# Kernel optimization log

Measured on AMD Instinct MI355X. Metric: run time of the kernel, lower is better.

The kernel has to match this reference:

```python
import jax, jax.numpy as jnp
import numpy as np

B, C, V = 65536, 2, 3          # batch of coords, coord_dim, value_dim
D, K, S = 64, 1024, 4          # latent_dim, num_codes, num_latent_vectors (VQ stages)
H, L, F = 1024, 5, 25          # hidden_size, num_layers, num_freqs
IN = C * (2 * F + 1)           # 102: positional-encoded decoder input
COMMIT = 0.25


def setup_inputs() -> dict:
    key = jax.random.key(0)
    ks = jax.random.split(key, 12)
    coords = jax.random.uniform(ks[0], (B, C), jnp.float32, -1.0, 1.0)
    latents = jax.random.normal(ks[1], (1, S, D), jnp.float32)
    cb = jax.random.normal(ks[2], (S, K, D), jnp.float32)
    codebooks = cb / jnp.linalg.norm(cb, axis=-1, keepdims=True)  # unit-norm init as in module
    mod_W = jax.random.normal(ks[3], (L, D, H), jnp.float32) / np.sqrt(D)
    mod_b = jax.random.normal(ks[4], (L, H), jnp.float32) * 0.01
    dec_W0 = jax.random.normal(ks[5], (IN, H), jnp.float32) / np.sqrt(IN)
    dec_b0 = jax.random.normal(ks[6], (H,), jnp.float32) * 0.01
    dec_Wh = jax.random.normal(ks[7], (L - 1, H, H), jnp.float32) / np.sqrt(H)
    dec_bh = jax.random.normal(ks[8], (L - 1, H), jnp.float32) * 0.01
    dec_Wout = jax.random.normal(ks[9], (H, V), jnp.float32) / np.sqrt(H)
    dec_bout = jax.random.normal(ks[10], (V,), jnp.float32) * 0.01
    return dict(coords=coords, latent_idx=0, latents=latents, codebooks=codebooks,
                mod_W=mod_W, mod_b=mod_b, dec_W0=dec_W0, dec_b0=dec_b0,
                dec_Wh=dec_Wh, dec_bh=dec_bh, dec_Wout=dec_Wout, dec_bout=dec_bout)


def _vq(z, emb):
    # z: (1, D), emb: (K, D) -> squared-distance argmin + straight-through
    d = jnp.sum(z * z, axis=1, keepdims=True) - 2.0 * (z @ emb.T) + jnp.sum(emb * emb, axis=1)
    idx = jnp.argmin(d, axis=1)               # (1,)
    z_q = emb[idx]                            # (1, D)
    z_q_st = z_q + jax.lax.stop_gradient(z - z_q)   # fwd value == z, grad flows to embedding
    loss = COMMIT * jnp.mean((jax.lax.stop_gradient(z_q) - z) ** 2)
    return z_q_st, idx, loss


def reference(coords, latent_idx, latents, codebooks, mod_W, mod_b,
              dec_W0, dec_b0, dec_Wh, dec_bh, dec_Wout, dec_bout):
    img = latents[latent_idx]                 # (S, D)
    z_q_sum = jnp.zeros((1, D), coords.dtype)
    residual_target = jnp.zeros((1, D), coords.dtype)
    total_vq_loss = 0.0
    idxs = []
    for s in range(S):                        # residual VQ over fixed small #stages
        z_stage = img[s:s + 1]
        if s == 0:
            residual_target = z_stage
            z_cur = z_stage
        else:
            residual_target = residual_target + z_stage
            z_cur = residual_target - jax.lax.stop_gradient(z_q_sum)
        z_q_st, idx, l = _vq(z_cur, codebooks[s])
        z_q_sum = z_q_sum + z_q_st
        total_vq_loss = total_vq_loss + l
        idxs.append(idx)
    # modulation betas from the (same-for-all-rows) quantized latent; broadcast over B
    betas = jnp.einsum('od,ldh->loh', z_q_sum, mod_W) + mod_b[:, None, :]   # (L, 1, H)
    # positional encoding: [x, sin(pi*f0*x), cos(pi*f0*x), sin(pi*f1*x), ...]
    freqs = 2.0 ** jnp.arange(F, dtype=coords.dtype)
    ang = coords[:, None, :] * (freqs[None, :, None] * jnp.pi)              # (B, F, C)
    pe = jnp.concatenate(
        [coords, jnp.stack([jnp.sin(ang), jnp.cos(ang)], axis=2).reshape(coords.shape[0], -1)],
        axis=-1)                                                            # (B, IN)
    h = jax.nn.relu(pe @ dec_W0 + dec_b0 + betas[0])
    for i in range(L - 1):
        h = jax.nn.relu(h @ dec_Wh[i] + dec_bh[i] + betas[i + 1])
    values = h @ dec_Wout + dec_bout                                        # (B, V)
    return values, jnp.stack(idxs), total_vq_loss
```

## Files before the change

kernel.cpp:

```cpp
#include <hip/hip_runtime.h>
#include <hip/hip_bf16.h>
#include <stdint.h>

#define NB   65536
#define NC   2
#define NV   3
#define ND   64
#define NK   1024
#define NS   4
#define NH   1024
#define NL   5
#define NF   25
#define NIN  102
#define K0P  128

typedef float f32x4 __attribute__((ext_vector_type(4)));
typedef int   i32x4 __attribute__((ext_vector_type(4)));
typedef int   i32x8 __attribute__((ext_vector_type(8)));
typedef unsigned char u8;

__device__ __forceinline__ void load_lds16(const void* g, void* l) {
    __builtin_amdgcn_global_load_lds(
        (const __attribute__((address_space(1))) void*)g,
        (__attribute__((address_space(3))) void*)l,
        16, 0, 0);
}

__device__ __forceinline__ u8 to_fp8(float x) {
    return (u8)(__builtin_amdgcn_cvt_pk_fp8_f32(x, 0.0f, 0, false) & 0xff);
}


__global__ __launch_bounds__(1024) void vq_kernel(
    const float* __restrict__ latents, const int* __restrict__ latent_idx,
    const float* __restrict__ codebooks, float* __restrict__ zq_out,
    float* __restrict__ out) {
    __shared__ float zcur[ND], resid[ND], zqsum[ND], ssq[ND];
    __shared__ float sDw[16];
    __shared__ int   sKw[16];
    __shared__ int   sBest;
    int t = threadIdx.x, lane = t & 63, wv = t >> 6;
    const float* img = latents + (size_t)latent_idx[0] * (NS * ND);
    if (t < ND) { resid[t] = 0.f; zqsum[t] = 0.f; }
    __syncthreads();
    float lossAcc = 0.f;
    for (int s = 0; s < NS; s++) {
        if (t < ND) {
            float iv = img[s * ND + t];
            float r  = resid[t] + iv;
            resid[t] = r;
            zcur[t]  = (s == 0) ? iv : (r - zqsum[t]);
        }
        __syncthreads();
        float zz = 0.f;
#pragma unroll
        for (int d = 0; d < ND; d++) { float z = zcur[d]; zz += z * z; }
        const float4* e4 = (const float4*)(codebooks + ((size_t)s * NK + t) * ND);
        float dot = 0.f, ee = 0.f;
#pragma unroll
        for (int i = 0; i < 16; i++) {
            float4 v = e4[i];
            dot += zcur[4 * i + 0] * v.x; dot += zcur[4 * i + 1] * v.y;
            dot += zcur[4 * i + 2] * v.z; dot += zcur[4 * i + 3] * v.w;
            ee  += v.x * v.x; ee += v.y * v.y; ee += v.z * v.z; ee += v.w * v.w;
        }
        float dmin = zz - 2.0f * dot + ee;
        int   kmin = t;
#pragma unroll
        for (int m = 1; m < 64; m <<= 1) {
            float d2 = __shfl_xor(dmin, m);
            int   k2 = __shfl_xor(kmin, m);
            if (d2 < dmin || (d2 == dmin && k2 < kmin)) { dmin = d2; kmin = k2; }
        }
        if (lane == 0) { sDw[wv] = dmin; sKw[wv] = kmin; }
        __syncthreads();
        if (t == 0) {
            float bd = sDw[0]; int bk = sKw[0];
            for (int w = 1; w < 16; w++) {
                float d2 = sDw[w]; int k2 = sKw[w];
                if (d2 < bd || (d2 == bd && k2 < bk)) { bd = d2; bk = k2; }
            }
            sBest = bk;
            out[NB * NV + s] = (float)bk;
        }
        __syncthreads();
        int best = sBest;
        const float* eb = codebooks + ((size_t)s * NK + best) * ND;
        if (t < ND) {
            float zq = eb[t];
            float d  = zq - zcur[t];
            ssq[t]   = d * d;
            zqsum[t] = zqsum[t] + (zq + (zcur[t] - zq));
        }
        __syncthreads();
        if (t == 0) {
            float sum = 0.f;
            for (int d = 0; d < ND; d++) sum += ssq[d];
            lossAcc += 0.25f * (sum / (float)ND);
        }
    }
    if (t < ND) zq_out[t] = zqsum[t];
    if (t == 0) out[NB * NV + NS] = lossAcc;
}

__global__ __launch_bounds__(256) void betas_kernel(
    const float* __restrict__ zq, const float* __restrict__ mod_W,
    const float* __restrict__ mod_b, const float* __restrict__ b0,
    const float* __restrict__ bh, float* __restrict__ bb) {
    int g = blockIdx.x * 256 + threadIdx.x;
    int l = g >> 10, n = g & 1023;
    float acc = mod_b[g];
    for (int d = 0; d < ND; d++) acc += zq[d] * mod_W[(size_t)(l * ND + d) * NH + n];
    acc += (l == 0) ? b0[n] : bh[(size_t)(l - 1) * NH + n];
    bb[g] = acc;
}

__global__ __launch_bounds__(256) void init_out_kernel(
    const float* __restrict__ bout, float* __restrict__ out) {
    int g = blockIdx.x * 256 + threadIdx.x;
    out[g] = bout[g % NV];
}

__global__ __launch_bounds__(256) void prep_kernel(
    const float* __restrict__ src, u8* __restrict__ dst, int Ks, int Kp) {
    __shared__ float tile[32][33];
    int nIt = Kp >> 7;
    src += (size_t)blockIdx.z * Ks * NH;
    dst += (size_t)blockIdx.z * NH * Kp;
    int k0 = blockIdx.x * 32, n0 = blockIdx.y * 32;
    int tx = threadIdx.x, ty = threadIdx.y;
    for (int i = 0; i < 4; i++) {
        int k = k0 + ty + i * 8;
        int n = n0 + tx;
        tile[ty + i * 8][tx] = (k < Ks) ? src[(size_t)k * NH + n] : 0.0f;
    }
    __syncthreads();
    for (int i = 0; i < 4; i++) {
        int n = n0 + ty + i * 8;
        int k = k0 + tx;
        int bn = n >> 7, j = (n >> 4) & 7, r16 = n & 15;
        int it = k >> 7, q = (k >> 5) & 3, half = (k >> 4) & 1, b16 = k & 15;
        size_t flat = ((size_t)(((bn * nIt + it) * 8 + j) * 2 + half)) * 1024
                    + (q * 16 + r16) * 16 + b16;
        dst[flat] = to_fp8(tile[tx][ty + i * 8] * 64.0f);
    }
}

__device__ __forceinline__ float pe_val(const float* coords, int m, int k) {
    if (k < 2) return coords[m * 2 + k];
    if (k >= NIN) return 0.0f;
    int u = k - 2;
    int f = u >> 2, r = u & 3;
    float c = coords[m * 2 + (r & 1)];
    float a = c * __builtin_ldexpf(3.14159274101257324f, f);
    return (r < 2) ? sinf(a) : cosf(a);
}

__global__ __launch_bounds__(256) void pe_kernel(
    const float* __restrict__ coords, u8* __restrict__ pe) {
    int g = blockIdx.x * 256 + threadIdx.x;
    int m = g >> 5, k4 = (g & 31) * 4;
    float v0 = pe_val(coords, m, k4 + 0);
    float v1 = pe_val(coords, m, k4 + 1);
    float v2 = pe_val(coords, m, k4 + 2);
    float v3 = pe_val(coords, m, k4 + 3);
    int p = __builtin_amdgcn_cvt_pk_fp8_f32(v0, v1, 0, false);
    p     = __builtin_amdgcn_cvt_pk_fp8_f32(v2, v3, p, true);
    int m16 = m >> 4, r = m & 15, c32 = k4 >> 5, b = k4 & 31;
    *(int*)(pe + ((size_t)(m16 * 4 + c32) * 16 + r) * 32 + b) = p;
}

template <int MODE, int KT>
__global__ __launch_bounds__(256, 2) void gemm_kernel(
    const u8* __restrict__ A, const u8* __restrict__ W,
    const float* __restrict__ bb, u8* __restrict__ O,
    const float* __restrict__ Wout, float* __restrict__ out, int Mb) {
    __shared__ __align__(16) u8 smem[32768];
    u8* sW0 = smem;
    u8* sW1 = smem + 16384;
    int t   = threadIdx.x;
    int fid = blockIdx.x;
    int xcd = fid & 7;
    int j8  = fid >> 3;
    int bn  = j8 & 7;
    int bm  = xcd * (Mb >> 3) + (j8 >> 3);
    int lane = t & 63, wm = t >> 6;
    int q    = lane >> 4, r16 = lane & 15;
    const int nIt = KT >> 7;

    const u8* wslab = W + (size_t)(bn * nIt) * 16384;
    const u8* abase = A + ((size_t)(bm * 16 + wm * 4) * (KT >> 5)) * 512 + lane * 32;

    f32x4 acc[4][8];
    f32x4 zero = {0.f, 0.f, 0.f, 0.f};
    for (int i = 0; i < 4; i++)
        for (int j = 0; j < 8; j++) acc[i][j] = zero;

#pragma unroll
    for (int p = 0; p < 4; p++) {
        int g = p * 256 + t;
        load_lds16((const void*)(wslab + g * 16), (void*)(sW0 + g * 16));
    }
    i32x8 afc[4], afn[4];
#pragma unroll
    for (int i = 0; i < 4; i++) {
        const u8* p = abase + ((size_t)i * (KT >> 5)) * 512;
        i32x4 lo = *(const i32x4*)(p);
        i32x4 hi = *(const i32x4*)(p + 16);
        afc[i] = __builtin_shufflevector(lo, hi, 0, 1, 2, 3, 4, 5, 6, 7);
    }
    __syncthreads();

#pragma unroll 1
    for (int it = 0; it < nIt; it++) {
        u8* bufc = (it & 1) ? sW1 : sW0;
        u8* bufn = (it & 1) ? sW0 : sW1;
        if (it + 1 < nIt) {
            const u8* ws = wslab + (size_t)(it + 1) * 16384;
#pragma unroll
            for (int p = 0; p < 4; p++) {
                int g = p * 256 + t;
                load_lds16((const void*)(ws + g * 16), (void*)(bufn + g * 16));
            }
#pragma unroll
            for (int i = 0; i < 4; i++) {
                const u8* p = abase + ((size_t)i * (KT >> 5) + (it + 1) * 4) * 512;
                i32x4 lo = *(const i32x4*)(p);
                i32x4 hi = *(const i32x4*)(p + 16);
                afn[i] = __builtin_shufflevector(lo, hi, 0, 1, 2, 3, 4, 5, 6, 7);
            }
        }
#pragma unroll
        for (int j = 0; j < 8; j++) {
            i32x4 lo = *(const i32x4*)(bufc + j * 2048 + lane * 16);
            i32x4 hi = *(const i32x4*)(bufc + j * 2048 + 1024 + lane * 16);
            i32x8 bfr = __builtin_shufflevector(lo, hi, 0, 1, 2, 3, 4, 5, 6, 7);
#pragma unroll
            for (int i = 0; i < 4; i++)
                acc[i][j] = __builtin_amdgcn_mfma_scale_f32_16x16x128_f8f6f4(
                    bfr, afc[i], acc[i][j], 0, 0,
                    0, 0x79797979,
                    0, 0x7f7f7f7f);
        }
        __syncthreads();
#pragma unroll
        for (int i = 0; i < 4; i++) afc[i] = afn[i];
    }

    if constexpr (MODE == 0) {
        u8* eb = smem;
#pragma unroll
        for (int i = 0; i < 4; i++) {
#pragma unroll
            for (int j = 0; j < 8; j++) {
                int nl = j * 16 + q * 4;
                f32x4 b4 = *(const f32x4*)(bb + bn * 128 + nl);
                float v0 = fmaxf(acc[i][j][0] + b4[0], 0.0f);
                float v1 = fmaxf(acc[i][j][1] + b4[1], 0.0f);
                float v2 = fmaxf(acc[i][j][2] + b4[2], 0.0f);
                float v3 = fmaxf(acc[i][j][3] + b4[3], 0.0f);
                int p = __builtin_amdgcn_cvt_pk_fp8_f32(v0, v1, 0, false);
                p     = __builtin_amdgcn_cvt_pk_fp8_f32(v2, v3, p, true);
                int idx = (((wm * 4 + i) * 4 + (j >> 1)) * 16 + r16) * 32
                        + (j & 1) * 16 + q * 4;
                *(int*)(eb + idx) = p;
            }
        }
        __syncthreads();
#pragma unroll
        for (int rd = 0; rd < 8; rd++) {
            int g2  = rd * 256 + t;
            int seg = g2 >> 5, off = (g2 & 31) * 16;
            int m16l = seg >> 2, c32l = seg & 3;
            i32x4 v = *(const i32x4*)(eb + seg * 512 + off);
            *(i32x4*)(O + ((size_t)((bm * 16 + m16l) * 32 + bn * 4 + c32l)) * 512 + off) = v;
        }
    } else {
#pragma unroll
        for (int i = 0; i < 4; i++) {
            float p0 = 0.f, p1 = 0.f, p2 = 0.f;
#pragma unroll
            for (int j = 0; j < 8; j++) {
                int nb = bn * 128 + j * 16 + q * 4;
                f32x4 b4 = *(const f32x4*)(bb + nb);
#pragma unroll
                for (int r = 0; r < 4; r++) {
                    float val = fmaxf(acc[i][j][r] + b4[r], 0.0f);
                    const float* w = Wout + (size_t)(nb + r) * NV;
                    p0 += val * w[0]; p1 += val * w[1]; p2 += val * w[2];
                }
            }
            p0 += __shfl_xor(p0, 16); p0 += __shfl_xor(p0, 32);
            p1 += __shfl_xor(p1, 16); p1 += __shfl_xor(p1, 32);
            p2 += __shfl_xor(p2, 16); p2 += __shfl_xor(p2, 32);
            if (q == 0) {
                int m = bm * 256 + wm * 64 + i * 16 + r16;
                atomicAdd(&out[(size_t)m * NV + 0], p0);
                atomicAdd(&out[(size_t)m * NV + 1], p1);
                atomicAdd(&out[(size_t)m * NV + 2], p2);
            }
        }
    }
}

extern "C" void kernel_launch(void* const* d_in, const int* in_sizes, int n_in,
                              void* d_out, int out_size, void* d_ws, size_t ws_size,
                              hipStream_t stream) {
    const float* coords     = (const float*)d_in[0];
    const int*   latent_idx = (const int*)d_in[1];
    const float* latents    = (const float*)d_in[2];
    const float* codebooks  = (const float*)d_in[3];
    const float* mod_W      = (const float*)d_in[4];
    const float* mod_b      = (const float*)d_in[5];
    const float* dec_W0     = (const float*)d_in[6];
    const float* dec_b0     = (const float*)d_in[7];
    const float* dec_Wh     = (const float*)d_in[8];
    const float* dec_bh     = (const float*)d_in[9];
    const float* dec_Wout   = (const float*)d_in[10];
    const float* dec_bout   = (const float*)d_in[11];
    float* out = (float*)d_out;

    char* wsb = (char*)d_ws;
    float* zq  = (float*)(wsb + 0);
    float* bb  = (float*)(wsb + 256);
    u8*    W0T = (u8*)(wsb + 20736);
    u8*    WhT = (u8*)(wsb + 151808);
    const size_t fixed_end = 4346368;

    int Bc = 65536;
    while (Bc > 2048 && fixed_end + 2 * (size_t)Bc * NH > ws_size)
        Bc >>= 1;
    int Mb = Bc / 256;

    u8* hA = (u8*)(wsb + fixed_end);
    u8* hB = hA + (size_t)Bc * NH;
    u8* pe = hB;

    vq_kernel<<<1, 1024, 0, stream>>>(latents, latent_idx, codebooks, zq, out);
    betas_kernel<<<20, 256, 0, stream>>>(zq, mod_W, mod_b, dec_b0, dec_bh, bb);
    init_out_kernel<<<(NB * NV) / 256, 256, 0, stream>>>(dec_bout, out);
    prep_kernel<<<dim3(4, 32, 1), dim3(32, 8), 0, stream>>>(dec_W0, W0T, NIN, K0P);
    prep_kernel<<<dim3(32, 32, 4), dim3(32, 8), 0, stream>>>(dec_Wh, WhT, NH, NH);

    for (int c0 = 0; c0 < NB; c0 += Bc) {
        pe_kernel<<<(Bc * 32) / 256, 256, 0, stream>>>(coords + (size_t)c0 * NC, pe);
        gemm_kernel<0, K0P><<<8 * Mb, 256, 0, stream>>>(
            pe, W0T, bb + 0 * NH, hA, nullptr, nullptr, Mb);
        gemm_kernel<0, NH><<<8 * Mb, 256, 0, stream>>>(
            hA, WhT + 0 * (size_t)NH * NH, bb + 1 * NH, hB, nullptr, nullptr, Mb);
        gemm_kernel<0, NH><<<8 * Mb, 256, 0, stream>>>(
            hB, WhT + 1 * (size_t)NH * NH, bb + 2 * NH, hA, nullptr, nullptr, Mb);
        gemm_kernel<0, NH><<<8 * Mb, 256, 0, stream>>>(
            hA, WhT + 2 * (size_t)NH * NH, bb + 3 * NH, hB, nullptr, nullptr, Mb);
        gemm_kernel<1, NH><<<8 * Mb, 256, 0, stream>>>(
            hB, WhT + 3 * (size_t)NH * NH, bb + 4 * NH, nullptr,
            dec_Wout, out + (size_t)c0 * NV, Mb);
    }
}
```

Before: 473.7 us.

## Switch decoder GEMMs from FP8 to FP4 operands with scaled MFMA

Quantizes weights, positional encodings and hidden activations to 4-bit E2M1 instead of FP8, and packs two values per byte with new layouts. The scaled MFMA now runs in FP4 mode with per-layer exponent scales. This halves the bytes moved for activations and weights and uses the faster FP4 matrix rate. The cost is much coarser quantization of the MLP, which may push accuracy past tolerance.

```diff
diff --git a/kernel.cpp b/kernel.cpp
--- a/kernel.cpp
+++ b/kernel.cpp
@@ -18,6 +18,8 @@
 typedef int   i32x4 __attribute__((ext_vector_type(4)));
 typedef int   i32x8 __attribute__((ext_vector_type(8)));
 typedef unsigned char u8;
+typedef unsigned short u16;
+typedef unsigned int u32;
 
 __device__ __forceinline__ void load_lds16(const void* g, void* l) {
     __builtin_amdgcn_global_load_lds(
@@ -26,8 +28,19 @@
         16, 0, 0);
 }
 
-__device__ __forceinline__ u8 to_fp8(float x) {
-    return (u8)(__builtin_amdgcn_cvt_pk_fp8_f32(x, 0.0f, 0, false) & 0xff);
+__device__ __forceinline__ u32 to_fp4(float x) {
+    float ax = fabsf(x);
+    u32 s = (x < 0.0f) ? 8u : 0u;
+    u32 m;
+    if      (ax < 0.25f) m = 0;
+    else if (ax < 0.75f) m = 1;
+    else if (ax < 1.25f) m = 2;
+    else if (ax < 1.75f) m = 3;
+    else if (ax < 2.50f) m = 4;
+    else if (ax < 3.50f) m = 5;
+    else if (ax < 5.00f) m = 6;
+    else                 m = 7;
+    return s | m;
 }
 
 
@@ -122,28 +135,32 @@
 }
 
 __global__ __launch_bounds__(256) void prep_kernel(
-    const float* __restrict__ src, u8* __restrict__ dst, int Ks, int Kp) {
+    const float* __restrict__ src, u8* __restrict__ dst, int Ks, int Kp,
+    float presc) {
     __shared__ float tile[32][33];
     int nIt = Kp >> 7;
     src += (size_t)blockIdx.z * Ks * NH;
-    dst += (size_t)blockIdx.z * NH * Kp;
+    dst += (size_t)blockIdx.z * NH * (Kp >> 1);
     int k0 = blockIdx.x * 32, n0 = blockIdx.y * 32;
-    int tx = threadIdx.x, ty = threadIdx.y;
+    int tx = threadIdx.x & 31, ty = threadIdx.x >> 5;
     for (int i = 0; i < 4; i++) {
         int k = k0 + ty + i * 8;
         int n = n0 + tx;
         tile[ty + i * 8][tx] = (k < Ks) ? src[(size_t)k * NH + n] : 0.0f;
     }
     __syncthreads();
-    for (int i = 0; i < 4; i++) {
-        int n = n0 + ty + i * 8;
-        int k = k0 + tx;
-        int bn = n >> 7, j = (n >> 4) & 7, r16 = n & 15;
-        int it = k >> 7, q = (k >> 5) & 3, half = (k >> 4) & 1, b16 = k & 15;
-        size_t flat = ((size_t)(((bn * nIt + it) * 8 + j) * 2 + half)) * 1024
-                    + (q * 16 + r16) * 16 + b16;
-        dst[flat] = to_fp8(tile[tx][ty + i * 8] * 64.0f);
-    }
+    int tid = threadIdx.x;
+    int n   = n0 + (tid >> 3);
+    int ks  = (tid & 7) * 4;
+    u32 n0b = to_fp4(tile[ks + 0][n - n0] * presc);
+    u32 n1b = to_fp4(tile[ks + 1][n - n0] * presc);
+    u32 n2b = to_fp4(tile[ks + 2][n - n0] * presc);
+    u32 n3b = to_fp4(tile[ks + 3][n - n0] * presc);
+    u16 us = (u16)((n0b | (n1b << 4)) | ((n2b | (n3b << 4)) << 8));
+    int it = k0 >> 7, q = (k0 >> 5) & 3;
+    int bn = n >> 7, j = (n >> 4) & 7, r16 = n & 15;
+    size_t flat = ((size_t)(((bn * nIt + it) * 8 + j) * 64 + q * 16 + r16)) * 16 + (ks >> 1);
+    *(u16*)(dst + flat) = us;
 }
 
 __device__ __forceinline__ float pe_val(const float* coords, int m, int k) {
@@ -159,25 +176,24 @@
 __global__ __launch_bounds__(256) void pe_kernel(
     const float* __restrict__ coords, u8* __restrict__ pe) {
     int g = blockIdx.x * 256 + threadIdx.x;
-    int m = g >> 5, k4 = (g & 31) * 4;
-    float v0 = pe_val(coords, m, k4 + 0);
-    float v1 = pe_val(coords, m, k4 + 1);
-    float v2 = pe_val(coords, m, k4 + 2);
-    float v3 = pe_val(coords, m, k4 + 3);
-    int p = __builtin_amdgcn_cvt_pk_fp8_f32(v0, v1, 0, false);
-    p     = __builtin_amdgcn_cvt_pk_fp8_f32(v2, v3, p, true);
-    int m16 = m >> 4, r = m & 15, c32 = k4 >> 5, b = k4 & 31;
-    *(int*)(pe + ((size_t)(m16 * 4 + c32) * 16 + r) * 32 + b) = p;
+    int m = g >> 4, k8 = (g & 15) * 8;
+    u32 w = 0;
+#pragma unroll
+    for (int e = 0; e < 8; e++)
+        w |= to_fp4(pe_val(coords, m, k8 + e) * 4.0f) << (4 * e);
+    int m16 = m >> 4, r = m & 15, c32 = k8 >> 5, b = (k8 & 31) >> 1;
+    *(u32*)(pe + ((size_t)(m16 * 4 + c32) * 16 + r) * 16 + b) = w;
 }
 
 template <int MODE, int KT>
 __global__ __launch_bounds__(256, 2) void gemm_kernel(
     const u8* __restrict__ A, const u8* __restrict__ W,
     const float* __restrict__ bb, u8* __restrict__ O,
-    const float* __restrict__ Wout, float* __restrict__ out, int Mb) {
-    __shared__ __align__(16) u8 smem[32768];
+    const float* __restrict__ Wout, float* __restrict__ out, int Mb,
+    u32 kwrep, u32 karep) {
+    __shared__ __align__(16) u8 smem[16384];
     u8* sW0 = smem;
-    u8* sW1 = smem + 16384;
+    u8* sW1 = smem + 8192;
     int t   = threadIdx.x;
     int fid = blockIdx.x;
     int xcd = fid & 7;
@@ -188,27 +204,26 @@
     int q    = lane >> 4, r16 = lane & 15;
     const int nIt = KT >> 7;
 
-    const u8* wslab = W + (size_t)(bn * nIt) * 16384;
-    const u8* abase = A + ((size_t)(bm * 16 + wm * 4) * (KT >> 5)) * 512 + lane * 32;
+    const u8* wslab = W + (size_t)(bn * nIt) * 8192;
+    const u8* abase = A + (size_t)(bm * 16 + wm * 4) * (KT >> 5) * 256
+                        + (size_t)q * 256 + r16 * 16;
 
     f32x4 acc[4][8];
     f32x4 zero = {0.f, 0.f, 0.f, 0.f};
     for (int i = 0; i < 4; i++)
         for (int j = 0; j < 8; j++) acc[i][j] = zero;
 
-#pragma unroll
-    for (int p = 0; p < 4; p++) {
+    i32x4 zed = {0, 0, 0, 0};
+
+#pragma unroll
+    for (int p = 0; p < 2; p++) {
         int g = p * 256 + t;
         load_lds16((const void*)(wslab + g * 16), (void*)(sW0 + g * 16));
     }
-    i32x8 afc[4], afn[4];
-#pragma unroll
-    for (int i = 0; i < 4; i++) {
-        const u8* p = abase + ((size_t)i * (KT >> 5)) * 512;
-        i32x4 lo = *(const i32x4*)(p);
-        i32x4 hi = *(const i32x4*)(p + 16);
-        afc[i] = __builtin_shufflevector(lo, hi, 0, 1, 2, 3, 4, 5, 6, 7);
-    }
+    i32x4 afc[4], afn[4];
+#pragma unroll
+    for (int i = 0; i < 4; i++)
+        afc[i] = *(const i32x4*)(abase + (size_t)i * (KT >> 5) * 256);
     __syncthreads();
 
 #pragma unroll 1
@@ -216,31 +231,28 @@
         u8* bufc = (it & 1) ? sW1 : sW0;
         u8* bufn = (it & 1) ? sW0 : sW1;
         if (it + 1 < nIt) {
-            const u8* ws = wslab + (size_t)(it + 1) * 16384;
-#pragma unroll
-            for (int p = 0; p < 4; p++) {
+            const u8* ws = wslab + (size_t)(it + 1) * 8192;
+#pragma unroll
+            for (int p = 0; p < 2; p++) {
                 int g = p * 256 + t;
                 load_lds16((const void*)(ws + g * 16), (void*)(bufn + g * 16));
             }
 #pragma unroll
+            for (int i = 0; i < 4; i++)
+                afn[i] = *(const i32x4*)(abase + ((size_t)i * (KT >> 5) + (it + 1) * 4) * 256);
+        }
+#pragma unroll
+        for (int j = 0; j < 8; j++) {
+            i32x4 wd = *(const i32x4*)(bufc + (j * 64 + lane) * 16);
+            i32x8 bfr = __builtin_shufflevector(wd, zed, 0, 1, 2, 3, 4, 5, 6, 7);
+#pragma unroll
             for (int i = 0; i < 4; i++) {
-                const u8* p = abase + ((size_t)i * (KT >> 5) + (it + 1) * 4) * 512;
-                i32x4 lo = *(const i32x4*)(p);
-                i32x4 hi = *(const i32x4*)(p + 16);
-                afn[i] = __builtin_shufflevector(lo, hi, 0, 1, 2, 3, 4, 5, 6, 7);
-            }
-        }
-#pragma unroll
-        for (int j = 0; j < 8; j++) {
-            i32x4 lo = *(const i32x4*)(bufc + j * 2048 + lane * 16);
-            i32x4 hi = *(const i32x4*)(bufc + j * 2048 + 1024 + lane * 16);
-            i32x8 bfr = __builtin_shufflevector(lo, hi, 0, 1, 2, 3, 4, 5, 6, 7);
-#pragma unroll
-            for (int i = 0; i < 4; i++)
+                i32x8 af = __builtin_shufflevector(afc[i], zed, 0, 1, 2, 3, 4, 5, 6, 7);
                 acc[i][j] = __builtin_amdgcn_mfma_scale_f32_16x16x128_f8f6f4(
-                    bfr, afc[i], acc[i][j], 0, 0,
-                    0, 0x79797979,
-                    0, 0x7f7f7f7f);
+                    bfr, af, acc[i][j], 4, 4,
+                    0, (int)kwrep,
+                    0, (int)karep);
+            }
         }
         __syncthreads();
 #pragma unroll
@@ -252,28 +264,32 @@
 #pragma unroll
         for (int i = 0; i < 4; i++) {
 #pragma unroll
-            for (int j = 0; j < 8; j++) {
-                int nl = j * 16 + q * 4;
-                f32x4 b4 = *(const f32x4*)(bb + bn * 128 + nl);
-                float v0 = fmaxf(acc[i][j][0] + b4[0], 0.0f);
-                float v1 = fmaxf(acc[i][j][1] + b4[1], 0.0f);
-                float v2 = fmaxf(acc[i][j][2] + b4[2], 0.0f);
-                float v3 = fmaxf(acc[i][j][3] + b4[3], 0.0f);
-                int p = __builtin_amdgcn_cvt_pk_fp8_f32(v0, v1, 0, false);
-                p     = __builtin_amdgcn_cvt_pk_fp8_f32(v2, v3, p, true);
-                int idx = (((wm * 4 + i) * 4 + (j >> 1)) * 16 + r16) * 32
-                        + (j & 1) * 16 + q * 4;
-                *(int*)(eb + idx) = p;
-            }
-        }
-        __syncthreads();
-#pragma unroll
-        for (int rd = 0; rd < 8; rd++) {
+            for (int b = 0; b < 4; b++) {
+                u16 us[2];
+#pragma unroll
+                for (int h = 0; h < 2; h++) {
+                    int j  = 2 * b + h;
+                    int nl = j * 16 + q * 4;
+                    f32x4 b4 = *(const f32x4*)(bb + bn * 128 + nl);
+                    u32 n0b = to_fp4(fmaxf(acc[i][j][0] + b4[0], 0.0f) * 0.5f);
+                    u32 n1b = to_fp4(fmaxf(acc[i][j][1] + b4[1], 0.0f) * 0.5f);
+                    u32 n2b = to_fp4(fmaxf(acc[i][j][2] + b4[2], 0.0f) * 0.5f);
+                    u32 n3b = to_fp4(fmaxf(acc[i][j][3] + b4[3], 0.0f) * 0.5f);
+                    us[h] = (u16)((n0b | (n1b << 4)) | ((n2b | (n3b << 4)) << 8));
+                }
+                int rowb = (((wm * 4 + i) * 4 + b) * 16 + r16) * 16;
+                *(u16*)(eb + rowb + 2 * q)     = us[0];
+                *(u16*)(eb + rowb + 8 + 2 * q) = us[1];
+            }
+        }
+        __syncthreads();
+#pragma unroll
+        for (int rd = 0; rd < 4; rd++) {
             int g2  = rd * 256 + t;
-            int seg = g2 >> 5, off = (g2 & 31) * 16;
+            int seg = g2 >> 4, off = (g2 & 15) * 16;
             int m16l = seg >> 2, c32l = seg & 3;
-            i32x4 v = *(const i32x4*)(eb + seg * 512 + off);
-            *(i32x4*)(O + ((size_t)((bm * 16 + m16l) * 32 + bn * 4 + c32l)) * 512 + off) = v;
+            i32x4 v = *(const i32x4*)(eb + seg * 256 + off);
+            *(i32x4*)(O + ((size_t)((bm * 16 + m16l) * 32 + bn * 4 + c32l)) * 256 + off) = v;
         }
     } else {
 #pragma unroll
@@ -324,36 +340,42 @@
     float* zq  = (float*)(wsb + 0);
     float* bb  = (float*)(wsb + 256);
     u8*    W0T = (u8*)(wsb + 20736);
-    u8*    WhT = (u8*)(wsb + 151808);
-    const size_t fixed_end = 4346368;
+    u8*    WhT = (u8*)(wsb + 86272);
+    const size_t fixed_end = 2183424;
 
     int Bc = 65536;
-    while (Bc > 2048 && fixed_end + 2 * (size_t)Bc * NH > ws_size)
+    while (Bc > 2048 && fixed_end + (size_t)Bc * NH > ws_size)
         Bc >>= 1;
     int Mb = Bc / 256;
 
     u8* hA = (u8*)(wsb + fixed_end);
-    u8* hB = hA + (size_t)Bc * NH;
+    u8* hB = hA + (size_t)Bc * NH / 2;
     u8* pe = hB;
+
+    const u32 kw_h  = 122u * 0x01010101u;
+    const u32 kw_0  = 123u * 0x01010101u;
+    const u32 ka_pe = 125u * 0x01010101u;
+    const u32 ka_h  = 128u * 0x01010101u;
 
     vq_kernel<<<1, 1024, 0, stream>>>(latents, latent_idx, codebooks, zq, out);
     betas_kernel<<<20, 256, 0, stream>>>(zq, mod_W, mod_b, dec_b0, dec_bh, bb);
     init_out_kernel<<<(NB * NV) / 256, 256, 0, stream>>>(dec_bout, out);
-    prep_kernel<<<dim3(4, 32, 1), dim3(32, 8), 0, stream>>>(dec_W0, W0T, NIN, K0P);
-    prep_kernel<<<dim3(32, 32, 4), dim3(32, 8), 0, stream>>>(dec_Wh, WhT, NH, NH);
-
+    prep_kernel<<<dim3(4, 32, 1), 256, 0, stream>>>(dec_W0, W0T, NIN, K0P, 16.0f);
+    prep_kernel<<<dim3(32, 32, 4), 256, 0, stream>>>(dec_Wh, WhT, NH, NH, 32.0f);
+
+    const size_t whs = (size_t)NH * NH / 2;
     for (int c0 = 0; c0 < NB; c0 += Bc) {
-        pe_kernel<<<(Bc * 32) / 256, 256, 0, stream>>>(coords + (size_t)c0 * NC, pe);
+        pe_kernel<<<(Bc * 16) / 256, 256, 0, stream>>>(coords + (size_t)c0 * NC, pe);
         gemm_kernel<0, K0P><<<8 * Mb, 256, 0, stream>>>(
-            pe, W0T, bb + 0 * NH, hA, nullptr, nullptr, Mb);
+            pe, W0T, bb + 0 * NH, hA, nullptr, nullptr, Mb, kw_0, ka_pe);
         gemm_kernel<0, NH><<<8 * Mb, 256, 0, stream>>>(
-            hA, WhT + 0 * (size_t)NH * NH, bb + 1 * NH, hB, nullptr, nullptr, Mb);
+            hA, WhT + 0 * whs, bb + 1 * NH, hB, nullptr, nullptr, Mb, kw_h, ka_h);
         gemm_kernel<0, NH><<<8 * Mb, 256, 0, stream>>>(
-            hB, WhT + 1 * (size_t)NH * NH, bb + 2 * NH, hA, nullptr, nullptr, Mb);
+            hB, WhT + 1 * whs, bb + 2 * NH, hA, nullptr, nullptr, Mb, kw_h, ka_h);
         gemm_kernel<0, NH><<<8 * Mb, 256, 0, stream>>>(
-            hA, WhT + 2 * (size_t)NH * NH, bb + 3 * NH, hB, nullptr, nullptr, Mb);
+            hA, WhT + 2 * whs, bb + 3 * NH, hB, nullptr, nullptr, Mb, kw_h, ka_h);
         gemm_kernel<1, NH><<<8 * Mb, 256, 0, stream>>>(
-            hB, WhT + 3 * (size_t)NH * NH, bb + 4 * NH, nullptr,
-            dec_Wout, out + (size_t)c0 * NV, Mb);
-    }
-}
+            hB, WhT + 3 * whs, bb + 4 * NH, nullptr,
+            dec_Wout, out + (size_t)c0 * NV, Mb, kw_h, ka_h);
+    }
+}
```

New measurement: 571.2 us. 20.6% more time.
